# Performance work log

Measured on AMD Instinct MI355X. Metric: run time of the kernel, lower is better.

## Reference

```python
import jax, jax.numpy as jnp
import numpy as np

NBITS = 8          # attn_nbits
GROUP = 32         # per-group size along head_dim for Q/K quantizers
H = 16             # num_heads
EPS = 1e-8


def _ste(x, q):
    # straight-through estimator: forward=q, backward=identity
    return x + jax.lax.stop_gradient(q - x)


def pg_dynamic_quant(x, group_size=GROUP, nbits=NBITS):
    """Per-group symmetric dynamic fake-quant along last dim (ActPGDynamicQuantizer)."""
    qmax = 2.0 ** (nbits - 1) - 1
    lead, D = x.shape[:-1], x.shape[-1]
    xg = x.reshape(*lead, D // group_size, group_size)
    s = jnp.maximum(jnp.max(jnp.abs(xg), axis=-1, keepdims=True) / qmax, EPS)
    q = jnp.clip(jnp.round(xg / s), -qmax - 1.0, qmax) * s
    return _ste(x, q.reshape(x.shape))


def dynamic_quant(x, axis=2, nbits=NBITS):
    """Symmetric dynamic fake-quant, scale shared along `axis` (ActDynamicQuantizer)."""
    qmax = 2.0 ** (nbits - 1) - 1
    s = jnp.maximum(jnp.max(jnp.abs(x), axis=axis, keepdims=True) / qmax, EPS)
    q = jnp.clip(jnp.round(x / s), -qmax - 1.0, qmax) * s
    return _ste(x, q)


def static_scale_quant(x, nbits=NBITS):
    """Unsigned static-scale fake-quant for softmax map in [0,1] (ActStaticScaleQuantizer)."""
    qmax = 2.0 ** nbits - 1
    q = jnp.clip(jnp.round(x * qmax), 0.0, qmax) / qmax
    return _ste(x, q)


def setup_inputs() -> dict:
    key = jax.random.key(0)
    ks = jax.random.split(key, 7)
    B, L, C = 4, 1024, 1024
    return {
        "x":         jax.random.normal(ks[0], (B, L, C), jnp.float32),
        "attn_bias": jax.random.normal(ks[1], (1, 1, L, L), jnp.float32) * 0.1,
        "w_qkv":     jax.random.normal(ks[2], (3 * C, C), jnp.float32) * 0.02,
        "q_bias":    jax.random.normal(ks[3], (C,), jnp.float32) * 0.02,
        "v_bias":    jax.random.normal(ks[4], (C,), jnp.float32) * 0.02,
        "w_proj":    jax.random.normal(ks[5], (C, C), jnp.float32) * 0.02,
        "b_proj":    jax.random.normal(ks[6], (C,), jnp.float32) * 0.02,
    }


def reference(x, attn_bias, w_qkv, q_bias, v_bias, w_proj, b_proj):
    B, L, C = x.shape
    D = C // H
    scale = D ** -0.5
    # qkv projection: bias-free linear + concat(q_bias, zeros_k, v_bias)
    bias = jnp.concatenate([q_bias, jnp.zeros_like(q_bias), v_bias])
    qkv = (x @ w_qkv.T + bias).reshape(B, L, 3, H, D)
    q, k, v = jnp.transpose(qkv, (2, 0, 3, 1, 4))  # each [B,H,L,D]
    # inline fake-quantization (MODE 0 inference path)
    qq = pg_dynamic_quant(q)
    kk = pg_dynamic_quant(k)
    vv = dynamic_quant(v, axis=2)
    attn = jnp.einsum('bhld,bhmd->bhlm', qq * scale, kk) + attn_bias  # [B,H,L,L]
    a = jax.nn.softmax(attn, axis=-1)
    a = static_scale_quant(a)
    out = jnp.einsum('bhlm,bhmd->bhld', a, vv)
    out = jnp.transpose(out, (0, 2, 1, 3)).reshape(B, L, C)
    return out @ w_proj.T + b_proj
```

## Files before the change

kernel.cpp:

```cpp
#include <hip/hip_runtime.h>


typedef unsigned short u16;
typedef unsigned int u32;
typedef __attribute__((ext_vector_type(8))) _Float16 half8;
typedef __attribute__((ext_vector_type(4))) float f32x4;
typedef __attribute__((ext_vector_type(4))) int i32x4;

__device__ __forceinline__ u16 f2b(float f) {
    u32 i;
    __builtin_memcpy(&i, &f, 4);
    return (u16)((i + 0x7FFFu + ((i >> 16) & 1u)) >> 16);
}

__device__ __forceinline__ void split16(float v, u16& hi, u16& lo) {
    _Float16 h = (_Float16)v;
    _Float16 l = (_Float16)(v - (float)h);
    __builtin_memcpy(&hi, &h, 2);
    __builtin_memcpy(&lo, &l, 2);
}

__device__ __forceinline__ int dot4(int a, int b, int c) {
#if __has_builtin(__builtin_amdgcn_sdot4)
    return __builtin_amdgcn_sdot4(a, b, c, false);
#else
    int r = c;
    r += ((a << 24) >> 24) * ((b << 24) >> 24);
    r += ((a << 16) >> 24) * ((b << 16) >> 24);
    r += ((a << 8) >> 24) * ((b << 8) >> 24);
    r += (a >> 24) * (b >> 24);
    return r;
#endif
}

__device__ __forceinline__ double fexp(double x) {
    double kd = rint(x * 1.4426950408889634);
    double r = fma(kd, -6.93147180369123816490e-01, x);
    r = fma(kd, -1.90821492927058770002e-10, r);
    double p = 2.7557319223985888e-07;
    p = fma(p, r, 2.7557319223985890e-06);
    p = fma(p, r, 2.4801587301587302e-05);
    p = fma(p, r, 1.9841269841269841e-04);
    p = fma(p, r, 1.3888888888888889e-03);
    p = fma(p, r, 8.3333333333333333e-03);
    p = fma(p, r, 4.1666666666666664e-02);
    p = fma(p, r, 1.6666666666666666e-01);
    p = fma(p, r, 0.5);
    p = fma(p, r, 1.0);
    p = fma(p, r, 1.0);
    long long bits;
    __builtin_memcpy(&bits, &p, 8);
    bits += ((long long)kd) << 52;
    double e;
    __builtin_memcpy(&e, &bits, 8);
    return (x < -700.0) ? 0.0 : e;
}

__global__ __launch_bounds__(256) void cvt_bf16w(u16* __restrict__ dst,
                                                 const float* __restrict__ src, int n) {
    int i = (blockIdx.x * 256 + threadIdx.x) * 4;
    if (i + 3 < n) {
        float4 v = *(const float4*)(src + i);
        ushort4 o;
        o.x = f2b(v.x); o.y = f2b(v.y); o.z = f2b(v.z); o.w = f2b(v.w);
        *(ushort4*)(dst + i) = o;
    }
}

__global__ __launch_bounds__(256) void gemm_qkv3(const float* __restrict__ A,
                                                 const float* __restrict__ Bm,
                                                 const float* __restrict__ qbias,
                                                 const float* __restrict__ vbias,
                                                 float* __restrict__ qws,
                                                 float* __restrict__ kws,
                                                 float* __restrict__ vws) {
    __shared__ u16 Ah[128 * 32], Al[128 * 32], Bh[64 * 32], Bl[64 * 32];
    const int t = threadIdx.x;
    const int lane = t & 63, w = t >> 6;
    const int srow = t >> 2, scol = (t & 3) * 8;
    const int lm = lane & 15, lk = (lane >> 4) * 8;
    const int bm = blockIdx.y, bn = blockIdx.x;

    const float* ap = A + (size_t)(bm * 128 + srow) * 1024 + scol;
    const float* bp = Bm + (size_t)(bn * 64 + srow) * 1024 + scol;

    double dacc[2][4][4];
#pragma unroll
    for (int i = 0; i < 2; i++)
#pragma unroll
        for (int j = 0; j < 4; j++)
#pragma unroll
            for (int r = 0; r < 4; r++) dacc[i][j][r] = 0.0;

    for (int slab = 0; slab < 8; slab++) {
        f32x4 acc[2][4];
#pragma unroll
        for (int i = 0; i < 2; i++)
#pragma unroll
            for (int j = 0; j < 4; j++) acc[i][j] = (f32x4){0.f, 0.f, 0.f, 0.f};

        for (int kc = 0; kc < 4; kc++) {
            const int k0 = slab * 128 + kc * 32;
            float vreg[3][8];
#pragma unroll
            for (int e = 0; e < 3; e++) {
                const float* src = (e < 2) ? (ap + e * (size_t)64 * 1024 + k0)
                                           : (bp + k0);
                float4 v0 = *(const float4*)(src);
                float4 v1 = *(const float4*)(src + 4);
                vreg[e][0] = v0.x; vreg[e][1] = v0.y; vreg[e][2] = v0.z; vreg[e][3] = v0.w;
                vreg[e][4] = v1.x; vreg[e][5] = v1.y; vreg[e][6] = v1.z; vreg[e][7] = v1.w;
            }
            __syncthreads();
#pragma unroll
            for (int e = 0; e < 3; e++) {
                union { u16 us[8]; uint4 v; } ph, pl;
#pragma unroll
                for (int j = 0; j < 8; j++) split16(vreg[e][j], ph.us[j], pl.us[j]);
                u16* dh = (e < 2) ? Ah : Bh;
                u16* dl = (e < 2) ? Al : Bl;
                int row = (e < 2) ? (srow + e * 64) : srow;
                *(uint4*)(dh + row * 32 + scol) = ph.v;
                *(uint4*)(dl + row * 32 + scol) = pl.v;
            }
            __syncthreads();

            half8 fah[2], fal[2], fbh[4], fbl[4];
#pragma unroll
            for (int i = 0; i < 2; i++) {
                int ra = (w * 32 + i * 16 + lm) * 32 + lk;
                fah[i] = *(const half8*)(Ah + ra);
                fal[i] = *(const half8*)(Al + ra);
            }
#pragma unroll
            for (int i = 0; i < 4; i++) {
                int rb = (i * 16 + lm) * 32 + lk;
                fbh[i] = *(const half8*)(Bh + rb);
                fbl[i] = *(const half8*)(Bl + rb);
            }
#pragma unroll
            for (int mi = 0; mi < 2; mi++)
#pragma unroll
                for (int ni = 0; ni < 4; ni++) {
                    acc[mi][ni] = __builtin_amdgcn_mfma_f32_16x16x32_f16(
                        fal[mi], fbh[ni], acc[mi][ni], 0, 0, 0);
                    acc[mi][ni] = __builtin_amdgcn_mfma_f32_16x16x32_f16(
                        fah[mi], fbl[ni], acc[mi][ni], 0, 0, 0);
                    acc[mi][ni] = __builtin_amdgcn_mfma_f32_16x16x32_f16(
                        fah[mi], fbh[ni], acc[mi][ni], 0, 0, 0);
                }
        }
#pragma unroll
        for (int i = 0; i < 2; i++)
#pragma unroll
            for (int j = 0; j < 4; j++)
#pragma unroll
                for (int r = 0; r < 4; r++) dacc[i][j][r] += (double)acc[i][j][r];
    }

    const int rbase = bm * 128 + w * 32 + (lane >> 4) * 4;
    const int cbase = bn * 64 + lm;
#pragma unroll
    for (int mi = 0; mi < 2; mi++)
#pragma unroll
        for (int ni = 0; ni < 4; ni++) {
            int col = cbase + ni * 16;
            int sel = col >> 10, cc = col & 1023;
            double bias = (sel == 0) ? (double)qbias[cc]
                        : ((sel == 2) ? (double)vbias[cc] : 0.0);
            float* dst = (sel == 0) ? qws : ((sel == 1) ? kws : vws);
#pragma unroll
            for (int r = 0; r < 4; r++) {
                int row = rbase + mi * 16 + r;
                dst[(size_t)row * 1024 + cc] = (float)(dacc[mi][ni][r] + bias);
            }
        }
}

__global__ __launch_bounds__(256) void quant_qk(const float* __restrict__ pre,
                                                signed char* __restrict__ qout,
                                                double* __restrict__ sout) {
    size_t g = (size_t)blockIdx.x * 256 + threadIdx.x;
    const float* p = pre + g * 32;
    float v[32];
    float amax = 0.f;
#pragma unroll
    for (int i = 0; i < 8; i++) {
        float4 q4 = ((const float4*)p)[i];
        v[i * 4 + 0] = q4.x; v[i * 4 + 1] = q4.y; v[i * 4 + 2] = q4.z; v[i * 4 + 3] = q4.w;
        amax = fmaxf(amax, fmaxf(fmaxf(fabsf(q4.x), fabsf(q4.y)),
                                 fmaxf(fabsf(q4.z), fabsf(q4.w))));
    }
    double s = fmax((double)amax / 127.0, 1e-8);
    sout[g] = s;
    int pk[8];
#pragma unroll
    for (int i = 0; i < 8; i++) {
        int b0 = (int)fmin(fmax(rint((double)v[i * 4 + 0] / s), -128.0), 127.0);
        int b1 = (int)fmin(fmax(rint((double)v[i * 4 + 1] / s), -128.0), 127.0);
        int b2 = (int)fmin(fmax(rint((double)v[i * 4 + 2] / s), -128.0), 127.0);
        int b3 = (int)fmin(fmax(rint((double)v[i * 4 + 3] / s), -128.0), 127.0);
        pk[i] = (b0 & 255) | ((b1 & 255) << 8) | ((b2 & 255) << 16) | ((b3 & 255) << 24);
    }
    int4* d = (int4*)(qout + g * 32);
    d[0] = make_int4(pk[0], pk[1], pk[2], pk[3]);
    d[1] = make_int4(pk[4], pk[5], pk[6], pk[7]);
}

__global__ __launch_bounds__(256) void quant_k(const float* __restrict__ pre,
                                               int* __restrict__ kT,
                                               double* __restrict__ ksT) {
    size_t g = (size_t)blockIdx.x * 256 + threadIdx.x;
    const float* p = pre + g * 32;
    float v[32];
    float amax = 0.f;
#pragma unroll
    for (int i = 0; i < 8; i++) {
        float4 q4 = ((const float4*)p)[i];
        v[i * 4 + 0] = q4.x; v[i * 4 + 1] = q4.y; v[i * 4 + 2] = q4.z; v[i * 4 + 3] = q4.w;
        amax = fmaxf(amax, fmaxf(fmaxf(fabsf(q4.x), fabsf(q4.y)),
                                 fmaxf(fabsf(q4.z), fabsf(q4.w))));
    }
    double s = fmax((double)amax / 127.0, 1e-8);
    int pk[8];
#pragma unroll
    for (int i = 0; i < 8; i++) {
        int b0 = (int)fmin(fmax(rint((double)v[i * 4 + 0] / s), -128.0), 127.0);
        int b1 = (int)fmin(fmax(rint((double)v[i * 4 + 1] / s), -128.0), 127.0);
        int b2 = (int)fmin(fmax(rint((double)v[i * 4 + 2] / s), -128.0), 127.0);
        int b3 = (int)fmin(fmax(rint((double)v[i * 4 + 3] / s), -128.0), 127.0);
        pk[i] = (b0 & 255) | ((b1 & 255) << 8) | ((b2 & 255) << 16) | ((b3 & 255) << 24);
    }
    const int m = (int)((g >> 5) & 1023);
    const int b = (int)(g >> 15);
    const int sub = (int)(g & 31);
    const int h = sub >> 1, pp = sub & 1;
    const int bh = b * 16 + h;
    int* dst = kT + ((size_t)bh * 16 + pp * 8) * 1024 + m;
#pragma unroll
    for (int i = 0; i < 8; i++) dst[i * 1024] = pk[i];
    ksT[((size_t)bh * 2 + pp) * 1024 + m] = s;
}

__global__ __launch_bounds__(256) void vmax_part(const float* __restrict__ vws,
                                                 float* __restrict__ pmax) {
    const int lc = blockIdx.x, b = blockIdx.y, t = threadIdx.x;
#pragma unroll
    for (int j = 0; j < 4; j++) {
        int cc = t + j * 256;
        float mx = 0.f;
        for (int l = 0; l < 16; l++)
            mx = fmaxf(mx, fabsf(vws[((size_t)(b * 1024 + lc * 16 + l)) * 1024 + cc]));
        pmax[(size_t)(b * 64 + lc) * 1024 + cc] = mx;
    }
}

__global__ __launch_bounds__(256) void vmax_final(const float* __restrict__ pmax,
                                                  double* __restrict__ vs) {
    int id = blockIdx.x * 256 + threadIdx.x;
    int b = id >> 10, cc = id & 1023;
    float mx = 0.f;
    for (int p = 0; p < 64; p++)
        mx = fmaxf(mx, pmax[(size_t)(b * 64 + p) * 1024 + cc]);
    vs[id] = fmax((double)mx / 127.0, 1e-8);
}

__global__ __launch_bounds__(256) void vquant_t(const float* __restrict__ vraw,
                                                const double* __restrict__ vs,
                                                signed char* __restrict__ ivt) {
    const int mt = blockIdx.x;
    const int ccg = blockIdx.y;
    const int b = blockIdx.z;
    const int cc = ccg * 256 + threadIdx.x;
    const double s = vs[b * 1024 + cc];
    const float* src = vraw + ((size_t)(b * 1024) + mt * 16) * 1024 + cc;
    signed char bytes[16];
#pragma unroll
    for (int i = 0; i < 16; i++) {
        float v = src[(size_t)i * 1024];
        bytes[i] = (signed char)(int)fmin(fmax(rint((double)v / s), -128.0), 127.0);
    }
    int4 pk;
    __builtin_memcpy(&pk, bytes, 16);
    *(int4*)(ivt + ((size_t)(b * 1024) + cc) * 1024 + mt * 16) = pk;
}

__global__ __launch_bounds__(256) void colsum_k(const signed char* __restrict__ ivt,
                                                int* __restrict__ csum) {
    int id = blockIdx.x * 256 + threadIdx.x;
    const int4* p = (const int4*)(ivt + (size_t)id * 1024);
    int s = 0;
    for (int i = 0; i < 64; i++) {
        int4 w = p[i];
        s = dot4(w.x, 0x01010101, s);
        s = dot4(w.y, 0x01010101, s);
        s = dot4(w.z, 0x01010101, s);
        s = dot4(w.w, 0x01010101, s);
    }
    csum[id] = s;
}

__global__ __launch_bounds__(256) void attn_f(const signed char* __restrict__ qint,
                                              const int* __restrict__ kT,
                                              const double* __restrict__ qs,
                                              const double* __restrict__ ksT,
                                              const signed char* __restrict__ ivt,
                                              const double* __restrict__ vs,
                                              const int* __restrict__ csum,
                                              const float* __restrict__ abias,
                                              u16* __restrict__ ctx) {
    __shared__ __align__(16) char smem[36864];
    int*         kTs  = (int*)smem;
    double*      ks0s = (double*)(smem + 16384);
    double*      ks1s = (double*)(smem + 18432);
    signed char* Pl   = (signed char*)(smem + 20480);
    char*        Bv   = smem;

    const int t = threadIdx.x;
    const int wv = t >> 6, lane = t & 63;
    const int qt = blockIdx.x, h = blockIdx.y, b = blockIdx.z;
    const int bh = b * 16 + h;
    const int* kTg = kT + (size_t)bh * 16384;
    const double* ks0g = ksT + (size_t)(bh * 2) * 1024;
    const double* ks1g = ksT + (size_t)(bh * 2 + 1) * 1024;

    for (int rr = 0; rr < 4; rr++) {
        const int prow = rr * 4 + wv;
        const int row = qt * 16 + prow;
        const size_t qrow = (size_t)(b * 1024 + row);

        const int* qv = (const int*)(qint + qrow * 1024 + h * 64);
        int qd[16];
#pragma unroll
        for (int j = 0; j < 4; j++) {
            int4 tmp = ((const int4*)qv)[j];
            qd[j * 4 + 0] = tmp.x; qd[j * 4 + 1] = tmp.y;
            qd[j * 4 + 2] = tmp.z; qd[j * 4 + 3] = tmp.w;
        }
        const double sq0 = qs[qrow * 32 + 2 * h], sq1 = qs[qrow * 32 + 2 * h + 1];
        const float* ab = abias + (size_t)row * 1024;

        double sd[16];
        for (int c = 0; c < 4; c++) {
            __syncthreads();
#pragma unroll
            for (int r = 0; r < 4; r++) {
                const int j = wv * 4 + r;
                int4 val = *(const int4*)(kTg + (size_t)j * 1024 + c * 256 + 4 * lane);
                *(int4*)(&kTs[j * 256 + 4 * lane]) = val;
            }
            ks0s[t] = ks0g[c * 256 + t];
            ks1s[t] = ks1g[c * 256 + t];
            __syncthreads();
#pragma unroll
            for (int s = 0; s < 4; s++) {
                const int ml = s * 64 + lane;
                int I0 = 0, I1 = 0;
#pragma unroll
                for (int j = 0; j < 8; j++)  I0 = dot4(qd[j], kTs[j * 256 + ml], I0);
#pragma unroll
                for (int j = 8; j < 16; j++) I1 = dot4(qd[j], kTs[j * 256 + ml], I1);
                sd[c * 4 + s] = 0.125 * (sq0 * ks0s[ml] * (double)I0
                                       + sq1 * ks1s[ml] * (double)I1)
                              + (double)ab[c * 256 + ml];
            }
        }

        double mx = sd[0];
#pragma unroll
        for (int it = 1; it < 16; it++) mx = fmax(mx, sd[it]);
#pragma unroll
        for (int off = 1; off < 64; off <<= 1) mx = fmax(mx, __shfl_xor(mx, off));
        double sum = 0.0;
#pragma unroll
        for (int it = 0; it < 16; it++) {
            double e = fexp(sd[it] - mx);
            sd[it] = e;
            sum += e;
        }
#pragma unroll
        for (int off = 1; off < 64; off <<= 1) sum += __shfl_xor(sum, off);
        const double inv = 1.0 / sum;

        const int xr = prow << 3;
        signed char* pr = Pl + prow * 1024;
#pragma unroll
        for (int it = 0; it < 16; it++) {
            double a = sd[it] * inv;
            double nd = fmin(fmax(rint(a * 255.0), 0.0), 255.0);
            int ni = (int)nd;
            pr[(it * 64 + lane) ^ xr] = (signed char)(ni - 128);
        }
    }

    const int col = lane & 15;
    const int cc = h * 64 + wv * 16 + col;
    const signed char* bg = ivt + ((size_t)(b * 1024) + h * 64) * 1024;
    const int arow = lane & 15;
    const int xa = arow << 3;
    const int browo = (wv * 16 + col) * 128;
    const int xb = col << 3;
    const int kq = (lane >> 4) * 8;

    i32x4 acc = (i32x4){0, 0, 0, 0};
    for (int kc = 0; kc < 8; kc++) {
        __syncthreads();
        {
            const int vrow = t >> 2, seg = (t & 3) * 32;
            const signed char* src = bg + (size_t)vrow * 1024 + kc * 128 + seg;
            ulonglong2 q0 = *(const ulonglong2*)(src);
            ulonglong2 q1 = *(const ulonglong2*)(src + 16);
            const int xv = (vrow & 15) << 3;
            char* drow = Bv + vrow * 128;
            *(unsigned long long*)(drow + ((seg +  0) ^ xv)) = q0.x;
            *(unsigned long long*)(drow + ((seg +  8) ^ xv)) = q0.y;
            *(unsigned long long*)(drow + ((seg + 16) ^ xv)) = q1.x;
            *(unsigned long long*)(drow + ((seg + 24) ^ xv)) = q1.y;
        }
        __syncthreads();
#pragma unroll
        for (int ks = 0; ks < 4; ks++) {
            const int ko = ks * 32 + kq;
            long a, bvv;
            __builtin_memcpy(&a,   Pl + arow * 1024 + ((kc * 128 + ko) ^ xa), 8);
            __builtin_memcpy(&bvv, Bv + browo + (ko ^ xb), 8);
            acc = __builtin_amdgcn_mfma_i32_16x16x32_i8(a, bvv, acc, 0, 0, 0);
        }
    }

    const double sc = vs[b * 1024 + cc] * (1.0 / 255.0);
    const int cs = 128 * csum[b * 1024 + cc];
    const int rbase = qt * 16 + (lane >> 4) * 4;
#pragma unroll
    for (int r = 0; r < 4; r++) {
        int S = acc[r] + cs;
        double val = (double)S * sc;
        ctx[((size_t)(b * 1024) + rbase + r) * 1024 + cc] = f2b((float)val);
    }
}

__global__ __launch_bounds__(256) void gemm_proj(const u16* __restrict__ ctx,
                                                 const u16* __restrict__ wproj,
                                                 const float* __restrict__ bproj,
                                                 float* __restrict__ out) {
    typedef __attribute__((ext_vector_type(8))) short short8;
    __shared__ u16 As[128 * 32], Bs[128 * 32];
    f32x4 acc[4][4];
#pragma unroll
    for (int i = 0; i < 4; i++)
#pragma unroll
        for (int j = 0; j < 4; j++) acc[i][j] = (f32x4){0.f, 0.f, 0.f, 0.f};

    const int t = threadIdx.x;
    const int lane = t & 63, w = t >> 6;
    const int wm = w >> 1, wn = w & 1;
    const int srow = t >> 2, scol = (t & 3) * 8;
    const int lm = lane & 15, lk = (lane >> 4) * 8;
    const int bm = blockIdx.y, bn = blockIdx.x;
    const u16* ap = ctx + (size_t)(bm * 128 + srow) * 1024 + scol;
    const u16* bp = wproj + (size_t)(bn * 128 + srow) * 1024 + scol;

    for (int k0 = 0; k0 < 1024; k0 += 32) {
        uint4 a0 = *(const uint4*)(ap + k0);
        uint4 a1 = *(const uint4*)(ap + (size_t)64 * 1024 + k0);
        uint4 b0 = *(const uint4*)(bp + k0);
        uint4 b1 = *(const uint4*)(bp + (size_t)64 * 1024 + k0);
        __syncthreads();
        *(uint4*)(As + srow * 32 + scol) = a0;
        *(uint4*)(As + (srow + 64) * 32 + scol) = a1;
        *(uint4*)(Bs + srow * 32 + scol) = b0;
        *(uint4*)(Bs + (srow + 64) * 32 + scol) = b1;
        __syncthreads();
        short8 af[4], bfr[4];
#pragma unroll
        for (int i = 0; i < 4; i++) {
            af[i]  = *(const short8*)(As + (wm * 64 + i * 16 + lm) * 32 + lk);
            bfr[i] = *(const short8*)(Bs + (wn * 64 + i * 16 + lm) * 32 + lk);
        }
#pragma unroll
        for (int mi = 0; mi < 4; mi++)
#pragma unroll
            for (int ni = 0; ni < 4; ni++)
                acc[mi][ni] = __builtin_amdgcn_mfma_f32_16x16x32_bf16(
                    af[mi], bfr[ni], acc[mi][ni], 0, 0, 0);
    }

    const int rbase = bm * 128 + wm * 64 + (lane >> 4) * 4;
    const int cbase = bn * 128 + wn * 64 + lm;
#pragma unroll
    for (int mi = 0; mi < 4; mi++)
#pragma unroll
        for (int ni = 0; ni < 4; ni++) {
            int col = cbase + ni * 16;
            float bias = bproj[col];
#pragma unroll
            for (int r = 0; r < 4; r++) {
                int row = rbase + mi * 16 + r;
                out[(size_t)row * 1024 + col] = acc[mi][ni][r] + bias;
            }
        }
}

extern "C" void kernel_launch(void* const* d_in, const int* in_sizes, int n_in,
                              void* d_out, int out_size, void* d_ws, size_t ws_size,
                              hipStream_t stream) {
    const float* x     = (const float*)d_in[0];
    const float* abias = (const float*)d_in[1];
    const float* wqkv  = (const float*)d_in[2];
    const float* qbias = (const float*)d_in[3];
    const float* vbias = (const float*)d_in[4];
    const float* wproj = (const float*)d_in[5];
    const float* bproj = (const float*)d_in[6];
    float* out = (float*)d_out;

    char* ws = (char*)d_ws;
    float*       qpre    = (float*)(ws + 0);
    float*       kpre    = (float*)(ws + 16777216);
    float*       vraw    = (float*)(ws + 33554432);
    u16*         wprojbf = (u16*)  (ws + 50331648);
    signed char* qint    = (signed char*)(ws + 52428800);
    int*         kT      = (int*)  (ws + 56623104);
    double*      qs      = (double*)(ws + 60817408);
    double*      ksT     = (double*)(ws + 61865984);
    double*      vs      = (double*)(ws + 62914560);
    float*       pmax    = (float*)(ws + 62947328);
    u16*         ctx     = (u16*)(ws + 0);
    signed char* ivt     = (signed char*)(ws + 16777216);
    int*         csum    = (int*)(ws + 62947328);

    cvt_bf16w<<<1024, 256, 0, stream>>>(wprojbf, wproj, 1048576);
    gemm_qkv3<<<dim3(48, 32), 256, 0, stream>>>(x, wqkv, qbias, vbias,
                                                qpre, kpre, vraw);
    quant_qk<<<512, 256, 0, stream>>>(qpre, qint, qs);
    quant_k<<<512, 256, 0, stream>>>(kpre, kT, ksT);
    vmax_part<<<dim3(64, 4), 256, 0, stream>>>(vraw, pmax);
    vmax_final<<<16, 256, 0, stream>>>(pmax, vs);
    vquant_t<<<dim3(64, 4, 4), 256, 0, stream>>>(vraw, vs, ivt);
    colsum_k<<<16, 256, 0, stream>>>(ivt, csum);
    attn_f<<<dim3(64, 16, 4), 256, 0, stream>>>(qint, kT, qs, ksT, ivt, vs,
                                                csum, abias, ctx);
    gemm_proj<<<dim3(8, 32), 256, 0, stream>>>(ctx, wprojbf, bproj, out);
}
```

Measured before the change: 539.9 us.

## Presplit x into fp16 hi/lo and split attention into score and AV kernels

```diff
diff --git a/kernel.cpp b/kernel.cpp
--- a/kernel.cpp
+++ b/kernel.cpp
@@ -56,6 +56,22 @@
     return (x < -700.0) ? 0.0 : e;
 }
 
+__global__ __launch_bounds__(256) void presplit(const float* __restrict__ src,
+                                                u16* __restrict__ dh,
+                                                u16* __restrict__ dl, int n) {
+    int i = (blockIdx.x * 256 + threadIdx.x) * 4;
+    if (i + 3 < n) {
+        float4 v = *(const float4*)(src + i);
+        ushort4 h, l;
+        split16(v.x, h.x, l.x);
+        split16(v.y, h.y, l.y);
+        split16(v.z, h.z, l.z);
+        split16(v.w, h.w, l.w);
+        *(ushort4*)(dh + i) = h;
+        *(ushort4*)(dl + i) = l;
+    }
+}
+
 __global__ __launch_bounds__(256) void cvt_bf16w(u16* __restrict__ dst,
                                                  const float* __restrict__ src, int n) {
     int i = (blockIdx.x * 256 + threadIdx.x) * 4;
@@ -67,13 +83,14 @@
     }
 }
 
-__global__ __launch_bounds__(256) void gemm_qkv3(const float* __restrict__ A,
-                                                 const float* __restrict__ Bm,
-                                                 const float* __restrict__ qbias,
-                                                 const float* __restrict__ vbias,
-                                                 float* __restrict__ qws,
-                                                 float* __restrict__ kws,
-                                                 float* __restrict__ vws) {
+__global__ __launch_bounds__(256) void gemm_qkv3n(const u16* __restrict__ Ahg,
+                                                  const u16* __restrict__ Alg,
+                                                  const float* __restrict__ Bm,
+                                                  const float* __restrict__ qbias,
+                                                  const float* __restrict__ vbias,
+                                                  float* __restrict__ qws,
+                                                  float* __restrict__ kws,
+                                                  float* __restrict__ vws) {
     __shared__ u16 Ah[128 * 32], Al[128 * 32], Bh[64 * 32], Bl[64 * 32];
     const int t = threadIdx.x;
     const int lane = t & 63, w = t >> 6;
@@ -81,7 +98,8 @@
     const int lm = lane & 15, lk = (lane >> 4) * 8;
     const int bm = blockIdx.y, bn = blockIdx.x;
 
-    const float* ap = A + (size_t)(bm * 128 + srow) * 1024 + scol;
+    const u16* aph = Ahg + (size_t)(bm * 128 + srow) * 1024 + scol;
+    const u16* apl = Alg + (size_t)(bm * 128 + srow) * 1024 + scol;
     const float* bp = Bm + (size_t)(bn * 64 + srow) * 1024 + scol;
 
     double dacc[2][4][4];
@@ -101,27 +119,28 @@
 
         for (int kc = 0; kc < 4; kc++) {
             const int k0 = slab * 128 + kc * 32;
-            float vreg[3][8];
-#pragma unroll
-            for (int e = 0; e < 3; e++) {
-                const float* src = (e < 2) ? (ap + e * (size_t)64 * 1024 + k0)
-                                           : (bp + k0);
-                float4 v0 = *(const float4*)(src);
-                float4 v1 = *(const float4*)(src + 4);
-                vreg[e][0] = v0.x; vreg[e][1] = v0.y; vreg[e][2] = v0.z; vreg[e][3] = v0.w;
-                vreg[e][4] = v1.x; vreg[e][5] = v1.y; vreg[e][6] = v1.z; vreg[e][7] = v1.w;
+            uint4 a0h = *(const uint4*)(aph + k0);
+            uint4 a1h = *(const uint4*)(aph + (size_t)64 * 1024 + k0);
+            uint4 a0l = *(const uint4*)(apl + k0);
+            uint4 a1l = *(const uint4*)(apl + (size_t)64 * 1024 + k0);
+            float wv[8];
+            {
+                float4 v0 = *(const float4*)(bp + k0);
+                float4 v1 = *(const float4*)(bp + k0 + 4);
+                wv[0] = v0.x; wv[1] = v0.y; wv[2] = v0.z; wv[3] = v0.w;
+                wv[4] = v1.x; wv[5] = v1.y; wv[6] = v1.z; wv[7] = v1.w;
             }
             __syncthreads();
-#pragma unroll
-            for (int e = 0; e < 3; e++) {
+            *(uint4*)(Ah + srow * 32 + scol) = a0h;
+            *(uint4*)(Ah + (srow + 64) * 32 + scol) = a1h;
+            *(uint4*)(Al + srow * 32 + scol) = a0l;
+            *(uint4*)(Al + (srow + 64) * 32 + scol) = a1l;
+            {
                 union { u16 us[8]; uint4 v; } ph, pl;
 #pragma unroll
-                for (int j = 0; j < 8; j++) split16(vreg[e][j], ph.us[j], pl.us[j]);
-                u16* dh = (e < 2) ? Ah : Bh;
-                u16* dl = (e < 2) ? Al : Bl;
-                int row = (e < 2) ? (srow + e * 64) : srow;
-                *(uint4*)(dh + row * 32 + scol) = ph.v;
-                *(uint4*)(dl + row * 32 + scol) = pl.v;
+                for (int j = 0; j < 8; j++) split16(wv[j], ph.us[j], pl.us[j]);
+                *(uint4*)(Bh + srow * 32 + scol) = ph.v;
+                *(uint4*)(Bl + srow * 32 + scol) = pl.v;
             }
             __syncthreads();
 
@@ -300,97 +319,118 @@
     csum[id] = s;
 }
 
-__global__ __launch_bounds__(256) void attn_f(const signed char* __restrict__ qint,
-                                              const int* __restrict__ kT,
-                                              const double* __restrict__ qs,
-                                              const double* __restrict__ ksT,
-                                              const signed char* __restrict__ ivt,
-                                              const double* __restrict__ vs,
-                                              const int* __restrict__ csum,
-                                              const float* __restrict__ abias,
-                                              u16* __restrict__ ctx) {
-    __shared__ __align__(16) char smem[36864];
-    int*         kTs  = (int*)smem;
-    double*      ks0s = (double*)(smem + 16384);
-    double*      ks1s = (double*)(smem + 18432);
-    signed char* Pl   = (signed char*)(smem + 20480);
-    char*        Bv   = smem;
-
+__global__ __launch_bounds__(256) void attn_sc(const signed char* __restrict__ qint,
+                                               const int* __restrict__ kT,
+                                               const double* __restrict__ qs,
+                                               const double* __restrict__ ksT,
+                                               const float* __restrict__ abias,
+                                               signed char* __restrict__ Pp,
+                                               int b) {
+    __shared__ int    kTs[16][256];
+    __shared__ double ks0s[256], ks1s[256];
     const int t = threadIdx.x;
     const int wv = t >> 6, lane = t & 63;
-    const int qt = blockIdx.x, h = blockIdx.y, b = blockIdx.z;
+    const int qt = blockIdx.x, h = blockIdx.y;
+    const int row = qt * 4 + wv;
+    const size_t qrow = (size_t)(b * 1024 + row);
     const int bh = b * 16 + h;
+
+    const int* qv = (const int*)(qint + qrow * 1024 + h * 64);
+    int qd[16];
+#pragma unroll
+    for (int j = 0; j < 4; j++) {
+        int4 tmp = ((const int4*)qv)[j];
+        qd[j * 4 + 0] = tmp.x; qd[j * 4 + 1] = tmp.y;
+        qd[j * 4 + 2] = tmp.z; qd[j * 4 + 3] = tmp.w;
+    }
+    const double sq0 = qs[qrow * 32 + 2 * h], sq1 = qs[qrow * 32 + 2 * h + 1];
     const int* kTg = kT + (size_t)bh * 16384;
     const double* ks0g = ksT + (size_t)(bh * 2) * 1024;
     const double* ks1g = ksT + (size_t)(bh * 2 + 1) * 1024;
-
-    for (int rr = 0; rr < 4; rr++) {
-        const int prow = rr * 4 + wv;
-        const int row = qt * 16 + prow;
-        const size_t qrow = (size_t)(b * 1024 + row);
-
-        const int* qv = (const int*)(qint + qrow * 1024 + h * 64);
-        int qd[16];
-#pragma unroll
-        for (int j = 0; j < 4; j++) {
-            int4 tmp = ((const int4*)qv)[j];
-            qd[j * 4 + 0] = tmp.x; qd[j * 4 + 1] = tmp.y;
-            qd[j * 4 + 2] = tmp.z; qd[j * 4 + 3] = tmp.w;
-        }
-        const double sq0 = qs[qrow * 32 + 2 * h], sq1 = qs[qrow * 32 + 2 * h + 1];
-        const float* ab = abias + (size_t)row * 1024;
-
-        double sd[16];
-        for (int c = 0; c < 4; c++) {
-            __syncthreads();
-#pragma unroll
-            for (int r = 0; r < 4; r++) {
-                const int j = wv * 4 + r;
-                int4 val = *(const int4*)(kTg + (size_t)j * 1024 + c * 256 + 4 * lane);
-                *(int4*)(&kTs[j * 256 + 4 * lane]) = val;
-            }
-            ks0s[t] = ks0g[c * 256 + t];
-            ks1s[t] = ks1g[c * 256 + t];
-            __syncthreads();
-#pragma unroll
-            for (int s = 0; s < 4; s++) {
-                const int ml = s * 64 + lane;
-                int I0 = 0, I1 = 0;
-#pragma unroll
-                for (int j = 0; j < 8; j++)  I0 = dot4(qd[j], kTs[j * 256 + ml], I0);
-#pragma unroll
-                for (int j = 8; j < 16; j++) I1 = dot4(qd[j], kTs[j * 256 + ml], I1);
-                sd[c * 4 + s] = 0.125 * (sq0 * ks0s[ml] * (double)I0
-                                       + sq1 * ks1s[ml] * (double)I1)
-                              + (double)ab[c * 256 + ml];
-            }
-        }
-
-        double mx = sd[0];
-#pragma unroll
-        for (int it = 1; it < 16; it++) mx = fmax(mx, sd[it]);
-#pragma unroll
-        for (int off = 1; off < 64; off <<= 1) mx = fmax(mx, __shfl_xor(mx, off));
-        double sum = 0.0;
-#pragma unroll
-        for (int it = 0; it < 16; it++) {
-            double e = fexp(sd[it] - mx);
-            sd[it] = e;
-            sum += e;
-        }
-#pragma unroll
-        for (int off = 1; off < 64; off <<= 1) sum += __shfl_xor(sum, off);
-        const double inv = 1.0 / sum;
-
-        const int xr = prow << 3;
-        signed char* pr = Pl + prow * 1024;
-#pragma unroll
-        for (int it = 0; it < 16; it++) {
-            double a = sd[it] * inv;
-            double nd = fmin(fmax(rint(a * 255.0), 0.0), 255.0);
-            int ni = (int)nd;
-            pr[(it * 64 + lane) ^ xr] = (signed char)(ni - 128);
-        }
+    const float* ab = abias + (size_t)row * 1024;
+
+    double sd[16];
+    for (int c = 0; c < 4; c++) {
+        if (c) __syncthreads();
+#pragma unroll
+        for (int r = 0; r < 4; r++) {
+            const int j = wv * 4 + r;
+            int4 val = *(const int4*)(kTg + (size_t)j * 1024 + c * 256 + 4 * lane);
+            *(int4*)(&kTs[j][4 * lane]) = val;
+        }
+        ks0s[t] = ks0g[c * 256 + t];
+        ks1s[t] = ks1g[c * 256 + t];
+        __syncthreads();
+#pragma unroll
+        for (int s = 0; s < 4; s++) {
+            const int ml = s * 64 + lane;
+            int I0 = 0, I1 = 0;
+#pragma unroll
+            for (int j = 0; j < 8; j++)  I0 = dot4(qd[j], kTs[j][ml], I0);
+#pragma unroll
+            for (int j = 8; j < 16; j++) I1 = dot4(qd[j], kTs[j][ml], I1);
+            sd[c * 4 + s] = 0.125 * (sq0 * ks0s[ml] * (double)I0
+                                   + sq1 * ks1s[ml] * (double)I1)
+                          + (double)ab[c * 256 + ml];
+        }
+    }
+
+    double mx = sd[0];
+#pragma unroll
+    for (int it = 1; it < 16; it++) mx = fmax(mx, sd[it]);
+#pragma unroll
+    for (int off = 1; off < 64; off <<= 1) mx = fmax(mx, __shfl_xor(mx, off));
+    double sum = 0.0;
+#pragma unroll
+    for (int it = 0; it < 16; it++) {
+        double e = fexp(sd[it] - mx);
+        sd[it] = e;
+        sum += e;
+    }
+#pragma unroll
+    for (int off = 1; off < 64; off <<= 1) sum += __shfl_xor(sum, off);
+    const double inv = 1.0 / sum;
+
+    signed char* prow = Pp + ((size_t)h * 1024 + row) * 1024;
+#pragma unroll
+    for (int it = 0; it < 16; it++) {
+        double a = sd[it] * inv;
+        double nd = fmin(fmax(rint(a * 255.0), 0.0), 255.0);
+        int ni = (int)nd;
+        prow[it * 64 + lane] = (signed char)(ni - 128);
+    }
+}
+
+__global__ __launch_bounds__(256) void attn_av(const signed char* __restrict__ Pp,
+                                               const signed char* __restrict__ ivt,
+                                               const double* __restrict__ vs,
+                                               const int* __restrict__ csum,
+                                               u16* __restrict__ ctx,
+                                               int b) {
+    __shared__ __align__(16) char smem[24576];
+    signed char* Pl = (signed char*)smem;
+    char*        Bv = smem + 16384;
+    const int t = threadIdx.x;
+    const int wv = t >> 6, lane = t & 63;
+    const int qt = blockIdx.x, h = blockIdx.y;
+
+    {
+        const int row = t >> 4, seg = (t & 15) * 64;
+        const signed char* src = Pp + ((size_t)h * 1024 + qt * 16 + row) * 1024 + seg;
+        const int x = row << 3;
+        ulonglong2 q0 = *(const ulonglong2*)(src);
+        ulonglong2 q1 = *(const ulonglong2*)(src + 16);
+        ulonglong2 q2 = *(const ulonglong2*)(src + 32);
+        ulonglong2 q3 = *(const ulonglong2*)(src + 48);
+        signed char* dr = Pl + row * 1024;
+        *(unsigned long long*)(dr + ((seg +  0) ^ x)) = q0.x;
+        *(unsigned long long*)(dr + ((seg +  8) ^ x)) = q0.y;
+        *(unsigned long long*)(dr + ((seg + 16) ^ x)) = q1.x;
+        *(unsigned long long*)(dr + ((seg + 24) ^ x)) = q1.y;
+        *(unsigned long long*)(dr + ((seg + 32) ^ x)) = q2.x;
+        *(unsigned long long*)(dr + ((seg + 40) ^ x)) = q2.y;
+        *(unsigned long long*)(dr + ((seg + 48) ^ x)) = q3.x;
+        *(unsigned long long*)(dr + ((seg + 56) ^ x)) = q3.y;
     }
 
     const int col = lane & 15;
@@ -514,30 +554,37 @@
     float* out = (float*)d_out;
 
     char* ws = (char*)d_ws;
-    float*       qpre    = (float*)(ws + 0);
-    float*       kpre    = (float*)(ws + 16777216);
-    float*       vraw    = (float*)(ws + 33554432);
-    u16*         wprojbf = (u16*)  (ws + 50331648);
-    signed char* qint    = (signed char*)(ws + 52428800);
-    int*         kT      = (int*)  (ws + 56623104);
-    double*      qs      = (double*)(ws + 60817408);
-    double*      ksT     = (double*)(ws + 61865984);
-    double*      vs      = (double*)(ws + 62914560);
-    float*       pmax    = (float*)(ws + 62947328);
-    u16*         ctx     = (u16*)(ws + 0);
-    signed char* ivt     = (signed char*)(ws + 16777216);
-    int*         csum    = (int*)(ws + 62947328);
-
-    cvt_bf16w<<<1024, 256, 0, stream>>>(wprojbf, wproj, 1048576);
-    gemm_qkv3<<<dim3(48, 32), 256, 0, stream>>>(x, wqkv, qbias, vbias,
-                                                qpre, kpre, vraw);
+    const size_t M = 1048576;
+    u16*         xh      = (u16*)  (ws + 0);
+    u16*         xl      = (u16*)  (ws + 8 * M);
+    float*       qpre    = (float*)(ws + 16 * M);
+    float*       kpre    = (float*)(ws + 32 * M);
+    float*       vraw    = (float*)(ws + 48 * M);
+    signed char* qint    = (signed char*)(ws + 0);
+    int*         kT      = (int*)  (ws + 4 * M);
+    double*      qs      = (double*)(ws + 8 * M);
+    double*      ksT     = (double*)(ws + 9 * M);
+    double*      vs      = (double*)(ws + 10 * M);
+    u16*         wprojbf = (u16*)  (ws + 11 * M);
+    float*       pmax    = (float*)(ws + 13 * M);
+    int*         csum    = (int*)  (ws + 13 * M);
+    u16*         ctx     = (u16*)  (ws + 16 * M);
+    signed char* ivt     = (signed char*)(ws + 32 * M);
+    signed char* Pp      = (signed char*)(ws + 48 * M);
+
+    presplit<<<4096, 256, 0, stream>>>(x, xh, xl, 4194304);
+    gemm_qkv3n<<<dim3(48, 32), 256, 0, stream>>>(xh, xl, wqkv, qbias, vbias,
+                                                 qpre, kpre, vraw);
     quant_qk<<<512, 256, 0, stream>>>(qpre, qint, qs);
     quant_k<<<512, 256, 0, stream>>>(kpre, kT, ksT);
     vmax_part<<<dim3(64, 4), 256, 0, stream>>>(vraw, pmax);
     vmax_final<<<16, 256, 0, stream>>>(pmax, vs);
     vquant_t<<<dim3(64, 4, 4), 256, 0, stream>>>(vraw, vs, ivt);
     colsum_k<<<16, 256, 0, stream>>>(ivt, csum);
-    attn_f<<<dim3(64, 16, 4), 256, 0, stream>>>(qint, kT, qs, ksT, ivt, vs,
-                                                csum, abias, ctx);
+    cvt_bf16w<<<1024, 256, 0, stream>>>(wprojbf, wproj, 1048576);
+    for (int b = 0; b < 4; b++) {
+        attn_sc<<<dim3(256, 16), 256, 0, stream>>>(qint, kT, qs, ksT, abias, Pp, b);
+        attn_av<<<dim3(64, 16), 256, 0, stream>>>(Pp, ivt, vs, csum, ctx, b);
+    }
     gemm_proj<<<dim3(8, 32), 256, 0, stream>>>(ctx, wprojbf, bproj, out);
 }
```

New measurement: 716.9 us. 1.33x slower.
